# Optimization experiments

Measured on AMD Instinct MI355X. Metric: run time of the kernel, lower is better.

## Reference

```python
import jax, jax.numpy as jnp
import numpy as np

N, N_SPINS, N_HIDDEN = 8192, 1024, 1024


def setup_inputs() -> dict:
    key = jax.random.key(0)
    ks = jax.random.split(key, 6)
    s_in = 1.0 / np.sqrt(N_SPINS)
    s_h = 1.0 / np.sqrt(N_HIDDEN)
    return {
        "x": jax.random.normal(ks[0], (N, N_SPINS), dtype=jnp.float32),
        "W_in": jax.random.normal(ks[1], (N_HIDDEN, N_SPINS), dtype=jnp.float32) * s_in,
        "b_in": jax.random.normal(ks[2], (N_HIDDEN,), dtype=jnp.float32) * s_in,
        "Wq": jax.random.normal(ks[3], (N_HIDDEN, N_HIDDEN), dtype=jnp.float32) * s_h,
        "Wk": jax.random.normal(ks[4], (N_HIDDEN, N_HIDDEN), dtype=jnp.float32) * s_h,
        "Wv": jax.random.normal(ks[5], (N_HIDDEN, N_HIDDEN), dtype=jnp.float32) * s_h,
    }


def reference(x, W_in, b_in, Wq, Wk, Wv):
    # embedding: Linear(n_spins, n_hidden)  -> h: [N, H]
    h = x @ W_in.T + b_in
    q = h @ Wq.T                      # [N, H]
    k = h @ Wk.T                      # [N, H]
    v = h @ Wv.T                      # [N, H]
    scores = (q @ k.T) * 0.25         # [N, N], scale 1/4 as in source
    attn = jax.nn.softmax(scores, axis=0)  # softmax over dim=0 (columns)
    out = attn @ v                    # [N, H]
    # log(cosh(z)) = |z| + log1p(exp(-2|z|)) - log(2), numerically stable
    a = jnp.abs(out)
    logcosh = a + jnp.log1p(jnp.exp(-2.0 * a)) - jnp.log(jnp.asarray(2.0, out.dtype))
    return jnp.sum(logcosh, axis=-1)  # [N]
```

## Files before the change

kernel.cpp:

```cpp
#include <hip/hip_runtime.h>
#include <hip/hip_bf16.h>
#include <cstdint>
#include <cstddef>

#define NTOK 8192
#define NHID 1024

typedef __attribute__((ext_vector_type(8))) __bf16 bf16x8;
typedef __attribute__((ext_vector_type(4))) float f32x4;

__device__ __forceinline__ unsigned short f2bf(float f) {
    union { float f; unsigned u; } v; v.f = f;
    unsigned r = v.u + 0x7FFF + ((v.u >> 16) & 1);
    return (unsigned short)(r >> 16);
}

__device__ __forceinline__ float bf2f(unsigned short u) {
    union { unsigned u; float f; } v; v.u = ((unsigned)u) << 16;
    return v.f;
}

__device__ __forceinline__ void async_copy16(const void* gsrc, void* ldsdst) {
    __builtin_amdgcn_global_load_lds(
        (const __attribute__((address_space(1))) unsigned int*)gsrc,
        (__attribute__((address_space(3))) unsigned int*)ldsdst,
        16, 0, 0);
}

template <int EPI, bool SWAP>
__global__ __launch_bounds__(512, 2) void gemm_sq(
    const unsigned short* __restrict__ A,
    const unsigned short* __restrict__ B,
    void* __restrict__ C,
    const float* __restrict__ bias,
    float* __restrict__ zsum,
    float scale, int M, int N, int K, int lda, int ldb)
{
    __shared__ __attribute__((aligned(16))) unsigned short lds[2][32768];

    const int tid  = threadIdx.x;
    const int wave = tid >> 6;
    const int lane = tid & 63;
    const int bm = (SWAP ? blockIdx.x : blockIdx.y) * 256;
    const int bn = (SWAP ? blockIdx.y : blockIdx.x) * 256;
    const size_t ldaz = (size_t)lda;
    const size_t ldbz = (size_t)ldb;

    const int srow = lane >> 3;
    const int scol = ((lane & 7) ^ srow) * 8;
    const unsigned short* Ag[4];
    const unsigned short* Bg[4];
    int off[4];
#pragma unroll
    for (int t = 0; t < 4; ++t) {
        int r = (wave * 4 + t) * 8 + srow;
        Ag[t] = A + (size_t)(bm + r) * ldaz + scol;
        Bg[t] = B + (size_t)(bn + r) * ldbz + scol;
        off[t] = (wave * 4 + t) * 512;
    }

    const int wm = (wave >> 2) * 128;
    const int wn = (wave & 3) * 64;
    const int fr = lane & 15;
    const int frl = fr & 7;
    const int q = lane >> 4;

    const int pc0 = (q ^ frl) * 8;
    const int pc1 = ((4 + q) ^ frl) * 8;

    f32x4 acc[8][4] = {};

    const int nt = K >> 6;

    auto stageA = [&](int s) {
#pragma unroll
        for (int t = 0; t < 4; ++t) { async_copy16(Ag[t], &lds[s][off[t]]); Ag[t] += 64; }
    };
    auto stageB = [&](int s) {
#pragma unroll
        for (int t = 0; t < 4; ++t) { async_copy16(Bg[t], &lds[s][16384 + off[t]]); Bg[t] += 64; }
    };

    stageA(0);
    stageB(0);
    stageA(1);
    asm volatile("s_waitcnt vmcnt(4)" ::: "memory");
    asm volatile("s_barrier" ::: "memory");

    for (int t = 0; t < nt; ++t) {
        const int cb = t & 1;
        const unsigned short* As = &lds[cb][0];
        const unsigned short* Bs = &lds[cb][16384];

        if (t + 1 < nt) stageB(cb ^ 1);

        {
            bf16x8 a[8], b[4];
#pragma unroll
            for (int i = 0; i < 8; ++i)
                a[i] = *(const bf16x8*)&As[(wm + i * 16 + fr) * 64 + pc0];
#pragma unroll
            for (int j = 0; j < 4; ++j)
                b[j] = *(const bf16x8*)&Bs[(wn + j * 16 + fr) * 64 + pc0];
            __builtin_amdgcn_s_setprio(1);
#pragma unroll
            for (int i = 0; i < 8; ++i)
#pragma unroll
                for (int j = 0; j < 4; ++j)
                    acc[i][j] = __builtin_amdgcn_mfma_f32_16x16x32_bf16(
                        a[i], b[j], acc[i][j], 0, 0, 0);
            __builtin_amdgcn_s_setprio(0);
        }
        {
            bf16x8 a[8], b[4];
#pragma unroll
            for (int i = 0; i < 8; ++i)
                a[i] = *(const bf16x8*)&As[(wm + i * 16 + fr) * 64 + pc1];
#pragma unroll
            for (int j = 0; j < 4; ++j)
                b[j] = *(const bf16x8*)&Bs[(wn + j * 16 + fr) * 64 + pc1];
            __builtin_amdgcn_s_setprio(1);
#pragma unroll
            for (int i = 0; i < 8; ++i)
#pragma unroll
                for (int j = 0; j < 4; ++j)
                    acc[i][j] = __builtin_amdgcn_mfma_f32_16x16x32_bf16(
                        a[i], b[j], acc[i][j], 0, 0, 0);
            __builtin_amdgcn_s_setprio(0);
        }

        if (t + 1 < nt) {
            asm volatile("s_barrier" ::: "memory");
            if (t + 2 < nt) stageA(cb);
            if (t < nt - 2) asm volatile("s_waitcnt vmcnt(4)" ::: "memory");
            else            asm volatile("s_waitcnt vmcnt(0)" ::: "memory");
            asm volatile("s_barrier" ::: "memory");
        }
    }

    const int erow = q * 4;
#pragma unroll
    for (int j = 0; j < 4; ++j) {
        const int gcol = bn + wn + j * 16 + fr;
        const float bv = (EPI == 1 && bias) ? bias[gcol] : 0.0f;
        float colsum = 0.0f;
#pragma unroll
        for (int i = 0; i < 8; ++i) {
            const int grow0 = bm + wm + i * 16 + erow;
#pragma unroll
            for (int r = 0; r < 4; ++r) {
                float v;
                if (EPI == 2) {
                    v = __expf(fmaf(acc[i][j][r], scale, -64.0f));
                    colsum += v;
                } else {
                    v = acc[i][j][r] * scale + bv;
                }
                size_t idx = (size_t)(grow0 + r) * N + gcol;
                if (EPI == 0) ((float*)C)[idx] = v;
                else          ((unsigned short*)C)[idx] = f2bf(v);
            }
        }
        if (EPI == 2) {
            colsum += __shfl_xor(colsum, 16, 64);
            colsum += __shfl_xor(colsum, 32, 64);
            if (q == 0) atomicAdd(&zsum[gcol], colsum);
        }
    }
}

template <int EPI, bool SWAP>
__global__ __launch_bounds__(512, 2) void gemm_bt4(
    const unsigned short* __restrict__ A,
    const unsigned short* __restrict__ B,
    void* __restrict__ C,
    const float* __restrict__ bias,
    float* __restrict__ zsum,
    float scale, int M, int N, int K, int lda, int ldb)
{
    __shared__ __attribute__((aligned(16))) unsigned short lds[3][24576];

    const int tid  = threadIdx.x;
    const int wave = tid >> 6;
    const int lane = tid & 63;
    const int bm = (SWAP ? blockIdx.x : blockIdx.y) * 256;
    const int bn = (SWAP ? blockIdx.y : blockIdx.x) * 128;
    const size_t ldaz = (size_t)lda;
    const size_t ldbz = (size_t)ldb;

    const int srow = lane >> 3;
    const int scol = ((lane & 7) ^ srow) * 8;
    const unsigned short* Ag[4];
    const unsigned short* Bg[2];
    int Aoff[4], Boff[2];
#pragma unroll
    for (int t = 0; t < 4; ++t) {
        int r = (wave * 4 + t) * 8 + srow;
        Ag[t] = A + (size_t)(bm + r) * ldaz + scol;
        Aoff[t] = (wave * 4 + t) * 512;
    }
#pragma unroll
    for (int t = 0; t < 2; ++t) {
        int r = (wave * 2 + t) * 8 + srow;
        Bg[t] = B + (size_t)(bn + r) * ldbz + scol;
        Boff[t] = 16384 + (wave * 2 + t) * 512;
    }

    const int wm = (wave >> 1) * 64;
    const int wn = (wave & 1) * 64;
    const int fr = lane & 15;
    const int frl = fr & 7;
    const int q = lane >> 4;

    const int pc0 = (q ^ frl) * 8;
    const int pc1 = ((4 + q) ^ frl) * 8;

    f32x4 acc[4][4] = {};

    const int nt = K >> 6;

    {
        unsigned short* b0 = &lds[0][0];
        unsigned short* b1 = &lds[1][0];
#pragma unroll
        for (int u = 0; u < 4; ++u) { async_copy16(Ag[u], b0 + Aoff[u]); Ag[u] += 64; }
#pragma unroll
        for (int u = 0; u < 2; ++u) { async_copy16(Bg[u], b0 + Boff[u]); Bg[u] += 64; }
#pragma unroll
        for (int u = 0; u < 4; ++u) { async_copy16(Ag[u], b1 + Aoff[u]); Ag[u] += 64; }
#pragma unroll
        for (int u = 0; u < 2; ++u) { async_copy16(Bg[u], b1 + Boff[u]); Bg[u] += 64; }
        asm volatile("s_waitcnt vmcnt(6)" ::: "memory");
        asm volatile("s_barrier" ::: "memory");
    }

    bf16x8 a0_0, a0_1, a0_2, a0_3, b0_0, b0_1, b0_2, b0_3;
    bf16x8 a1_0, a1_1, a1_2, a1_3, b1_0, b1_1, b1_2, b1_3;

    {
        const unsigned short* As = &lds[0][0];
        const unsigned short* Bs = &lds[0][16384];
        a0_0 = *(const bf16x8*)&As[(wm +  0 + fr) * 64 + pc0];
        a0_1 = *(const bf16x8*)&As[(wm + 16 + fr) * 64 + pc0];
        a0_2 = *(const bf16x8*)&As[(wm + 32 + fr) * 64 + pc0];
        a0_3 = *(const bf16x8*)&As[(wm + 48 + fr) * 64 + pc0];
        b0_0 = *(const bf16x8*)&Bs[(wn +  0 + fr) * 64 + pc0];
        b0_1 = *(const bf16x8*)&Bs[(wn + 16 + fr) * 64 + pc0];
        b0_2 = *(const bf16x8*)&Bs[(wn + 32 + fr) * 64 + pc0];
        b0_3 = *(const bf16x8*)&Bs[(wn + 48 + fr) * 64 + pc0];
    }

#define MFMA16(AA0, AA1, AA2, AA3, BB0, BB1, BB2, BB3)                         \
    do {                                                                       \
        __builtin_amdgcn_s_setprio(1);                                         \
        acc[0][0] = __builtin_amdgcn_mfma_f32_16x16x32_bf16(AA0, BB0, acc[0][0], 0, 0, 0); \
        acc[0][1] = __builtin_amdgcn_mfma_f32_16x16x32_bf16(AA0, BB1, acc[0][1], 0, 0, 0); \
        acc[0][2] = __builtin_amdgcn_mfma_f32_16x16x32_bf16(AA0, BB2, acc[0][2], 0, 0, 0); \
        acc[0][3] = __builtin_amdgcn_mfma_f32_16x16x32_bf16(AA0, BB3, acc[0][3], 0, 0, 0); \
        acc[1][0] = __builtin_amdgcn_mfma_f32_16x16x32_bf16(AA1, BB0, acc[1][0], 0, 0, 0); \
        acc[1][1] = __builtin_amdgcn_mfma_f32_16x16x32_bf16(AA1, BB1, acc[1][1], 0, 0, 0); \
        acc[1][2] = __builtin_amdgcn_mfma_f32_16x16x32_bf16(AA1, BB2, acc[1][2], 0, 0, 0); \
        acc[1][3] = __builtin_amdgcn_mfma_f32_16x16x32_bf16(AA1, BB3, acc[1][3], 0, 0, 0); \
        acc[2][0] = __builtin_amdgcn_mfma_f32_16x16x32_bf16(AA2, BB0, acc[2][0], 0, 0, 0); \
        acc[2][1] = __builtin_amdgcn_mfma_f32_16x16x32_bf16(AA2, BB1, acc[2][1], 0, 0, 0); \
        acc[2][2] = __builtin_amdgcn_mfma_f32_16x16x32_bf16(AA2, BB2, acc[2][2], 0, 0, 0); \
        acc[2][3] = __builtin_amdgcn_mfma_f32_16x16x32_bf16(AA2, BB3, acc[2][3], 0, 0, 0); \
        acc[3][0] = __builtin_amdgcn_mfma_f32_16x16x32_bf16(AA3, BB0, acc[3][0], 0, 0, 0); \
        acc[3][1] = __builtin_amdgcn_mfma_f32_16x16x32_bf16(AA3, BB1, acc[3][1], 0, 0, 0); \
        acc[3][2] = __builtin_amdgcn_mfma_f32_16x16x32_bf16(AA3, BB2, acc[3][2], 0, 0, 0); \
        acc[3][3] = __builtin_amdgcn_mfma_f32_16x16x32_bf16(AA3, BB3, acc[3][3], 0, 0, 0); \
        __builtin_amdgcn_s_setprio(0);                                         \
    } while (0)

    int cb = 0;
    int sb = 2;
    for (int t = 0; t < nt; ++t) {
        const bool pf = (t + 2 < nt);
        const unsigned short* As = &lds[cb][0];
        const unsigned short* Bs = &lds[cb][16384];
        unsigned short* Sb = &lds[sb][0];
        const int nb = (cb == 2) ? 0 : cb + 1;
        const unsigned short* An = &lds[nb][0];
        const unsigned short* Bn = &lds[nb][16384];

        a1_0 = *(const bf16x8*)&As[(wm +  0 + fr) * 64 + pc1];
        a1_1 = *(const bf16x8*)&As[(wm + 16 + fr) * 64 + pc1];
        a1_2 = *(const bf16x8*)&As[(wm + 32 + fr) * 64 + pc1];
        a1_3 = *(const bf16x8*)&As[(wm + 48 + fr) * 64 + pc1];
        b1_0 = *(const bf16x8*)&Bs[(wn +  0 + fr) * 64 + pc1];
        b1_1 = *(const bf16x8*)&Bs[(wn + 16 + fr) * 64 + pc1];
        b1_2 = *(const bf16x8*)&Bs[(wn + 32 + fr) * 64 + pc1];
        b1_3 = *(const bf16x8*)&Bs[(wn + 48 + fr) * 64 + pc1];
        if (pf) {
#pragma unroll
            for (int u = 0; u < 4; ++u) { async_copy16(Ag[u], Sb + Aoff[u]); Ag[u] += 64; }
        }
        __builtin_amdgcn_sched_barrier(0);
        MFMA16(a0_0, a0_1, a0_2, a0_3, b0_0, b0_1, b0_2, b0_3);
        if (t < nt - 2) asm volatile("s_waitcnt vmcnt(4)" ::: "memory");
        else            asm volatile("s_waitcnt vmcnt(0)" ::: "memory");
        asm volatile("s_barrier" ::: "memory");

        if (t + 1 < nt) {
            a0_0 = *(const bf16x8*)&An[(wm +  0 + fr) * 64 + pc0];
            a0_1 = *(const bf16x8*)&An[(wm + 16 + fr) * 64 + pc0];
            a0_2 = *(const bf16x8*)&An[(wm + 32 + fr) * 64 + pc0];
            a0_3 = *(const bf16x8*)&An[(wm + 48 + fr) * 64 + pc0];
            b0_0 = *(const bf16x8*)&Bn[(wn +  0 + fr) * 64 + pc0];
            b0_1 = *(const bf16x8*)&Bn[(wn + 16 + fr) * 64 + pc0];
            b0_2 = *(const bf16x8*)&Bn[(wn + 32 + fr) * 64 + pc0];
            b0_3 = *(const bf16x8*)&Bn[(wn + 48 + fr) * 64 + pc0];
        }
        if (pf) {
#pragma unroll
            for (int u = 0; u < 2; ++u) { async_copy16(Bg[u], Sb + Boff[u]); Bg[u] += 64; }
        }
        __builtin_amdgcn_sched_barrier(0);
        MFMA16(a1_0, a1_1, a1_2, a1_3, b1_0, b1_1, b1_2, b1_3);
        asm volatile("s_barrier" ::: "memory");

        if (pf) sb = (sb == 2) ? 0 : sb + 1;
        cb = nb;
    }
#undef MFMA16

    const int erow = q * 4;
#pragma unroll
    for (int j = 0; j < 4; ++j) {
        const int gcol = bn + wn + j * 16 + fr;
        const float bv = (EPI == 1 && bias) ? bias[gcol] : 0.0f;
        float colsum = 0.0f;
#pragma unroll
        for (int i = 0; i < 4; ++i) {
            const int grow0 = bm + wm + i * 16 + erow;
#pragma unroll
            for (int r = 0; r < 4; ++r) {
                float v;
                if (EPI == 2) {
                    v = __expf(fmaf(acc[i][j][r], scale, -64.0f));
                    colsum += v;
                } else {
                    v = acc[i][j][r] * scale + bv;
                }
                size_t idx = (size_t)(grow0 + r) * N + gcol;
                if (EPI == 0) ((float*)C)[idx] = v;
                else          ((unsigned short*)C)[idx] = f2bf(v);
            }
        }
        if (EPI == 2) {
            colsum += __shfl_xor(colsum, 16, 64);
            colsum += __shfl_xor(colsum, 32, 64);
            if (q == 0) atomicAdd(&zsum[gcol], colsum);
        }
    }
}

__global__ void cvt_all(const float4* __restrict__ x,
                        const float4* __restrict__ w0,
                        const float4* __restrict__ w1,
                        const float4* __restrict__ w2,
                        const float4* __restrict__ w3,
                        ushort4* __restrict__ xb,
                        ushort4* __restrict__ wdst,
                        float4* __restrict__ pz4,
                        int n4x, int n4w)
{
    int i = blockIdx.x * blockDim.x + threadIdx.x;
    int n4 = n4x + 4 * n4w;
    if (i >= n4) {
        int zi = i - n4;
        if (zi < 2048) pz4[zi] = make_float4(0.f, 0.f, 0.f, 0.f);
        return;
    }
    float4 f;
    ushort4* dst;
    if (i < n4x) {
        f = x[i]; dst = xb + i;
    } else {
        int r = i - n4x;
        int seg = r / n4w, off = r % n4w;
        const float4* src = (seg == 0) ? w0 : (seg == 1) ? w1 : (seg == 2) ? w2 : w3;
        f = src[off]; dst = wdst + r;
    }
    ushort4 o;
    o.x = f2bf(f.x); o.y = f2bf(f.y); o.z = f2bf(f.z); o.w = f2bf(f.w);
    *dst = o;
}

__global__ __launch_bounds__(256) void transpose_scale(
    const unsigned short* __restrict__ v,
    const float* __restrict__ z,
    unsigned short* __restrict__ vt)
{
    __shared__ float lds[64 * 65];
    const int tid = threadIdx.x;
    const int j0 = blockIdx.x * 64;
    const int h0 = blockIdx.y * 64;
    const int c = tid & 63;
    const int r0 = tid >> 6;
#pragma unroll
    for (int it = 0; it < 16; ++it) {
        int r = it * 4 + r0;
        lds[r * 65 + c] = bf2f(v[(size_t)(j0 + r) * 3072 + h0 + c]);
    }
    __syncthreads();
    const float rz = 1.0f / z[j0 + c];
#pragma unroll
    for (int it = 0; it < 16; ++it) {
        int r = it * 4 + r0;
        vt[(size_t)(h0 + r) * NTOK + j0 + c] = f2bf(lds[c * 65 + r] * rz);
    }
}

__global__ void logcosh_rowsum(const ushort4* __restrict__ O4,
                               float* __restrict__ out)
{
    const float LN2 = 0.69314718055994531f;
    int row = blockIdx.x;
    ushort4 u = O4[(size_t)row * 256 + threadIdx.x];
    float s = 0.0f, a;
    a = fabsf(bf2f(u.x)); s += a + log1pf(__expf(-2.0f * a));
    a = fabsf(bf2f(u.y)); s += a + log1pf(__expf(-2.0f * a));
    a = fabsf(bf2f(u.z)); s += a + log1pf(__expf(-2.0f * a));
    a = fabsf(bf2f(u.w)); s += a + log1pf(__expf(-2.0f * a));
    s -= 4.0f * LN2;
    for (int off = 32; off; off >>= 1) s += __shfl_down(s, off, 64);
    __shared__ float red[4];
    if ((threadIdx.x & 63) == 0) red[threadIdx.x >> 6] = s;
    __syncthreads();
    if (threadIdx.x == 0) out[row] = red[0] + red[1] + red[2] + red[3];
}

extern "C" void kernel_launch(void* const* d_in, const int* in_sizes, int n_in,
                              void* d_out, int out_size, void* d_ws, size_t ws_size,
                              hipStream_t stream)
{
    (void)in_sizes; (void)n_in; (void)out_size; (void)ws_size;

    const float* x    = (const float*)d_in[0];
    const float* W_in = (const float*)d_in[1];
    const float* b_in = (const float*)d_in[2];
    const float* Wq   = (const float*)d_in[3];
    const float* Wk   = (const float*)d_in[4];
    const float* Wv   = (const float*)d_in[5];
    float* out = (float*)d_out;

    char* w = (char*)d_ws;
    const size_t MiB = 1024 * 1024;
    unsigned short* Pb     = (unsigned short*)(w);
    unsigned short* qkv    = (unsigned short*)(w + 128 * MiB);
    unsigned short* xb     = (unsigned short*)(w + 128 * MiB);
    unsigned short* outb   = (unsigned short*)(w + 128 * MiB);
    unsigned short* hb     = (unsigned short*)(w + 176 * MiB);
    unsigned short* vtb    = (unsigned short*)(w + 176 * MiB);
    unsigned short* wib    = (unsigned short*)(w + 192 * MiB);
    unsigned short* wqkvb  = (unsigned short*)(w + 194 * MiB);
    float*          pz     = (float*)         (w + 200 * MiB);

    {
        int n4x = NTOK * NHID / 4;
        int n4w = NHID * NHID / 4;
        int n4  = n4x + 4 * n4w;
        cvt_all<<<n4 / 256 + 8, 256, 0, stream>>>(
            (const float4*)x, (const float4*)W_in, (const float4*)Wq,
            (const float4*)Wk, (const float4*)Wv,
            (ushort4*)xb, (ushort4*)wib, (float4*)pz, n4x, n4w);
    }

    dim3 gNH(NHID / 128, NTOK / 256);
    gemm_bt4<1, false><<<gNH, 512, 0, stream>>>(
        xb, wib, hb, b_in, nullptr, 1.0f, NTOK, NHID, NHID, NHID, NHID);

    dim3 gQKV(3 * NHID / 128, NTOK / 256);
    gemm_bt4<1, false><<<gQKV, 512, 0, stream>>>(
        hb, wqkvb, qkv, nullptr, nullptr, 1.0f, NTOK, 3 * NHID, NHID, NHID, NHID);

    dim3 gS(NTOK / 256, NTOK / 256);
    gemm_sq<2, false><<<gS, 512, 0, stream>>>(
        qkv, qkv + NHID, Pb, nullptr, pz, 0.25f, NTOK, NTOK, NHID,
        3 * NHID, 3 * NHID);

    dim3 gT(NTOK / 64, NHID / 64);
    transpose_scale<<<gT, 256, 0, stream>>>(qkv + 2 * NHID, pz, vtb);

    dim3 gO(NTOK / 256, NHID / 128);
    gemm_bt4<1, true><<<gO, 512, 0, stream>>>(
        Pb, vtb, outb, nullptr, nullptr, 1.0f, NTOK, NHID, NTOK, NTOK, NTOK);

    logcosh_rowsum<<<NTOK, 256, 0, stream>>>((const ushort4*)outb, out);
}
```

Before: 474.6 us.

## Software-pipeline LDS fragment reads with MFMA in score GEMM

Restructures the score GEMM main loop so register fragments for the next half-K step are read from LDS while the MFMAs for the current fragments run. Two register fragment sets are used (ping-pong), with sched_barrier fences to stop the compiler from reordering the reads and MFMAs. This is meant to hide LDS read latency behind matrix math. In exchange it raises register pressure under the 512-thread, 2-block launch bound and could cause spills.

```diff
diff --git a/kernel.cpp b/kernel.cpp
--- a/kernel.cpp
+++ b/kernel.cpp
@@ -27,8 +27,31 @@
         16, 0, 0);
 }
 
+__device__ __forceinline__ void read_frags(
+    const unsigned short* __restrict__ As, const unsigned short* __restrict__ Bs,
+    int wm, int wn, int fr, int pc, bf16x8 (&a)[8], bf16x8 (&b)[4])
+{
+#pragma unroll
+    for (int i = 0; i < 8; ++i) a[i] = *(const bf16x8*)&As[(wm + i * 16 + fr) * 64 + pc];
+#pragma unroll
+    for (int j = 0; j < 4; ++j) b[j] = *(const bf16x8*)&Bs[(wn + j * 16 + fr) * 64 + pc];
+}
+
+__device__ __forceinline__ void mfma32(
+    const bf16x8 (&a)[8], const bf16x8 (&b)[4], f32x4 (&acc)[8][4])
+{
+    __builtin_amdgcn_s_setprio(1);
+#pragma unroll
+    for (int i = 0; i < 8; ++i)
+#pragma unroll
+        for (int j = 0; j < 4; ++j)
+            acc[i][j] = __builtin_amdgcn_mfma_f32_16x16x32_bf16(
+                a[i], b[j], acc[i][j], 0, 0, 0);
+    __builtin_amdgcn_s_setprio(0);
+}
+
 template <int EPI, bool SWAP>
-__global__ __launch_bounds__(512, 2) void gemm_sq(
+__global__ __launch_bounds__(512, 2) void gemm_sq2(
     const unsigned short* __restrict__ A,
     const unsigned short* __restrict__ B,
     void* __restrict__ C,
@@ -87,55 +110,31 @@
     asm volatile("s_waitcnt vmcnt(4)" ::: "memory");
     asm volatile("s_barrier" ::: "memory");
 
+    bf16x8 aP[8], bP[4];
+    bf16x8 aQ[8], bQ[4];
+    read_frags(&lds[0][0], &lds[0][16384], wm, wn, fr, pc0, aP, bP);
+
     for (int t = 0; t < nt; ++t) {
         const int cb = t & 1;
+        const int nb = cb ^ 1;
         const unsigned short* As = &lds[cb][0];
         const unsigned short* Bs = &lds[cb][16384];
 
-        if (t + 1 < nt) stageB(cb ^ 1);
-
-        {
-            bf16x8 a[8], b[4];
-#pragma unroll
-            for (int i = 0; i < 8; ++i)
-                a[i] = *(const bf16x8*)&As[(wm + i * 16 + fr) * 64 + pc0];
-#pragma unroll
-            for (int j = 0; j < 4; ++j)
-                b[j] = *(const bf16x8*)&Bs[(wn + j * 16 + fr) * 64 + pc0];
-            __builtin_amdgcn_s_setprio(1);
-#pragma unroll
-            for (int i = 0; i < 8; ++i)
-#pragma unroll
-                for (int j = 0; j < 4; ++j)
-                    acc[i][j] = __builtin_amdgcn_mfma_f32_16x16x32_bf16(
-                        a[i], b[j], acc[i][j], 0, 0, 0);
-            __builtin_amdgcn_s_setprio(0);
-        }
-        {
-            bf16x8 a[8], b[4];
-#pragma unroll
-            for (int i = 0; i < 8; ++i)
-                a[i] = *(const bf16x8*)&As[(wm + i * 16 + fr) * 64 + pc1];
-#pragma unroll
-            for (int j = 0; j < 4; ++j)
-                b[j] = *(const bf16x8*)&Bs[(wn + j * 16 + fr) * 64 + pc1];
-            __builtin_amdgcn_s_setprio(1);
-#pragma unroll
-            for (int i = 0; i < 8; ++i)
-#pragma unroll
-                for (int j = 0; j < 4; ++j)
-                    acc[i][j] = __builtin_amdgcn_mfma_f32_16x16x32_bf16(
-                        a[i], b[j], acc[i][j], 0, 0, 0);
-            __builtin_amdgcn_s_setprio(0);
-        }
-
-        if (t + 1 < nt) {
-            asm volatile("s_barrier" ::: "memory");
-            if (t + 2 < nt) stageA(cb);
-            if (t < nt - 2) asm volatile("s_waitcnt vmcnt(4)" ::: "memory");
-            else            asm volatile("s_waitcnt vmcnt(0)" ::: "memory");
-            asm volatile("s_barrier" ::: "memory");
-        }
+        if (t + 1 < nt) stageB(nb);
+        read_frags(As, Bs, wm, wn, fr, pc1, aQ, bQ);
+        __builtin_amdgcn_sched_barrier(0);
+        mfma32(aP, bP, acc);
+        asm volatile("s_waitcnt lgkmcnt(0)" ::: "memory");
+        asm volatile("s_barrier" ::: "memory");
+        if (t + 2 < nt) stageA(cb);
+        if (t < nt - 2) asm volatile("s_waitcnt vmcnt(4)" ::: "memory");
+        else            asm volatile("s_waitcnt vmcnt(0)" ::: "memory");
+        asm volatile("s_barrier" ::: "memory");
+
+        if (t + 1 < nt)
+            read_frags(&lds[nb][0], &lds[nb][16384], wm, wn, fr, pc0, aP, bP);
+        __builtin_amdgcn_sched_barrier(0);
+        mfma32(aQ, bQ, acc);
     }
 
     const int erow = q * 4;
@@ -476,7 +475,7 @@
         hb, wqkvb, qkv, nullptr, nullptr, 1.0f, NTOK, 3 * NHID, NHID, NHID, NHID);
 
     dim3 gS(NTOK / 256, NTOK / 256);
-    gemm_sq<2, false><<<gS, 512, 0, stream>>>(
+    gemm_sq2<2, false><<<gS, 512, 0, stream>>>(
         qkv, qkv + NHID, Pb, nullptr, pz, 0.25f, NTOK, NTOK, NHID,
         3 * NHID, 3 * NHID);
 
```

After: 487.2 us. 1.03x slower.
